# Performance work log

Hardware: AMD Instinct MI355X
Metric: run time of the kernel (lower is better)

## Reference

```python
import jax, jax.numpy as jnp
import numpy as np

NUM_HEADS = 8
SIZE_Q = 512
SIZE_K = 512
SIZE_V = 512
B, S = 2, 2048


def setup_inputs() -> dict:
    key = jax.random.key(0)
    ks = jax.random.split(key, 16)
    Hk = SIZE_K  # num_heads * head_size_k
    Hv = SIZE_V  # num_heads * head_size_v
    inp = {
        "k": jax.random.normal(ks[0], (B, S, SIZE_K), jnp.float32),
        "v": jax.random.normal(ks[1], (B, S, SIZE_V), jnp.float32),
        "q": jax.random.normal(ks[2], (B, S, SIZE_Q), jnp.float32),
        "mask": jax.random.randint(ks[3], (S, S), 0, 2).astype(jnp.bool_),
        "spatial_bias": jax.random.normal(ks[4], (1, NUM_HEADS, S, S), jnp.float32),
        # Linear params stored as [in, out]; y = x @ W + b
        "Wq": jax.random.normal(ks[5], (SIZE_Q, Hk), jnp.float32) / np.sqrt(SIZE_Q),
        "bq": jnp.zeros((Hk,), jnp.float32),
        "Wk": jax.random.normal(ks[6], (SIZE_K, Hk), jnp.float32) / np.sqrt(SIZE_K),
        "bk": jnp.zeros((Hk,), jnp.float32),
        "Wv": jax.random.normal(ks[7], (SIZE_V, Hv), jnp.float32) / np.sqrt(SIZE_V),
        "bv": jnp.zeros((Hv,), jnp.float32),
        "Wo": jax.random.normal(ks[8], (Hv, SIZE_V), jnp.float32) / np.sqrt(Hv),
        "bo": jnp.zeros((SIZE_V,), jnp.float32),
    }
    return inp


def reference(k, v, q, mask, spatial_bias, Wq, bq, Wk, bk, Wv, bv, Wo, bo):
    batch, sk = k.shape[0], k.shape[1]
    sq = q.shape[1]
    hdk = Wk.shape[1] // NUM_HEADS
    hdv = Wv.shape[1] // NUM_HEADS
    # QKV projections -> [B, H, S, hd]
    kp = (k @ Wk + bk).reshape(batch, sk, NUM_HEADS, hdk).transpose(0, 2, 1, 3)
    vp = (v @ Wv + bv).reshape(batch, sk, NUM_HEADS, hdv).transpose(0, 2, 1, 3)
    qp = (q @ Wq + bq).reshape(batch, sq, NUM_HEADS, hdk).transpose(0, 2, 1, 3)
    qp = qp / jnp.sqrt(jnp.asarray(hdk, qp.dtype))
    # Scores with additive spatial bias and boolean mask (2D mask -> [1,1,S,S])
    scores = jnp.einsum("bhqd,bhkd->bhqk", qp, kp) + spatial_bias
    scores = jnp.where(mask[None, None, :, :], scores, -jnp.inf)
    attn = jax.nn.softmax(scores, axis=-1)  # dropout=0 (eval)
    ctx = jnp.einsum("bhqk,bhkd->bhqd", attn, vp)
    ctx = ctx.transpose(0, 2, 1, 3).reshape(batch, sq, NUM_HEADS * hdv)
    return ctx @ Wo + bo
```

## Files before the change

### kernel.cpp

```cpp
#include <hip/hip_runtime.h>
#include <hip/hip_bf16.h>

#define S_LEN 2048
#define NH 8
#define HD 64
#define CH 512
#define NEG_BIG (-3.0e38f)

typedef __bf16 bf16;
typedef bf16 bf16x8 __attribute__((ext_vector_type(8)));
typedef bf16 bf16x4 __attribute__((ext_vector_type(4)));
typedef float floatx4 __attribute__((ext_vector_type(4)));

__global__ void detect_mask_kernel(const unsigned char* __restrict__ mb,
                                   int* __restrict__ flag_out) {
    __shared__ int s1, s3;
    if (threadIdx.x == 0) { s1 = 0; s3 = 0; }
    __syncthreads();
    int any1 = 0, any3 = 0;
    int base = threadIdx.x * 16;
    for (int i = base; i < base + 16; ++i) {
        unsigned char bch = mb[i];
        int m = i & 3;
        if (bch != 0) {
            if (m == 1) any1 = 1;
            if (m == 2 || m == 3) any3 = 1;
        }
    }
    if (any1) atomicOr(&s1, 1);
    if (any3) atomicOr(&s3, 1);
    __syncthreads();
    if (threadIdx.x == 0) {
        int f = 0;
        if (s1) f = 1;
        else if (s3) f = 2;
        *flag_out = f;
    }
}

__global__ __launch_bounds__(256) void prep_weights_kernel(
    const float* __restrict__ Wq, const float* __restrict__ Wk,
    const float* __restrict__ Wv, const float* __restrict__ Wo,
    bf16* __restrict__ WThi, bf16* __restrict__ WTlo)
{
    __shared__ float tile[64][65];
    const int t = threadIdx.x;
    const int n0 = blockIdx.x * 64;
    const int k0 = blockIdx.y * 64;
    const int mat = blockIdx.z;
    const float* W = (mat == 0) ? Wq : (mat == 1) ? Wk : (mat == 2) ? Wv : Wo;
    bf16* hi = WThi + (size_t)mat * (CH * CH);
    bf16* lo = WTlo + (size_t)mat * (CH * CH);
#pragma unroll
    for (int i = 0; i < 4; ++i) {
        int row = (t >> 4) + 16 * i;
        int c4 = (t & 15) << 2;
        float4 f = *(const float4*)(W + (size_t)(k0 + row) * CH + n0 + c4);
        tile[row][c4 + 0] = f.x; tile[row][c4 + 1] = f.y;
        tile[row][c4 + 2] = f.z; tile[row][c4 + 3] = f.w;
    }
    __syncthreads();
#pragma unroll
    for (int i = 0; i < 4; ++i) {
        int nr = (t >> 4) + 16 * i;
        int k4 = (t & 15) << 2;
        bf16x4 h, l;
#pragma unroll
        for (int j = 0; j < 4; ++j) {
            float x = tile[k4 + j][nr];
            bf16 hv = (bf16)x;
            h[j] = hv;
            l[j] = (bf16)(x - (float)hv);
        }
        *(bf16x4*)(hi + (size_t)(n0 + nr) * CH + k0 + k4) = h;
        *(bf16x4*)(lo + (size_t)(n0 + nr) * CH + k0 + k4) = l;
    }
}

__device__ __forceinline__ void gemm_bf16_tile(
    bf16* __restrict__ As_hi, bf16* __restrict__ As_lo,
    bf16* __restrict__ Bs_hi, bf16* __restrict__ Bs_lo,
    const float* __restrict__ IN, const bf16* __restrict__ WThi,
    const bf16* __restrict__ WTlo, const float* __restrict__ BI,
    float* __restrict__ OUT, float scale, int mode)
{
    const int t = threadIdx.x;
    const int w = t >> 6;
    const int lane = t & 63;
    const int m16 = lane & 15;
    const int quad = lane >> 4;
    const int m0 = blockIdx.y * 128;
    const int n0 = blockIdx.x * 128;

    const int arow = t >> 1;
    const int akc  = (t & 1) << 4;

    floatx4 acc[2][8];
#pragma unroll
    for (int mi = 0; mi < 2; ++mi)
#pragma unroll
        for (int ni = 0; ni < 8; ++ni) {
            acc[mi][ni][0] = 0.f; acc[mi][ni][1] = 0.f;
            acc[mi][ni][2] = 0.f; acc[mi][ni][3] = 0.f;
        }

    float4 af[4];
    bf16x8 pbh[2], pbl[2];

    auto loadA = [&](int k0) {
        const float* p = IN + (size_t)(m0 + arow) * CH + k0 + akc;
        af[0] = ((const float4*)p)[0];
        af[1] = ((const float4*)p)[1];
        af[2] = ((const float4*)p)[2];
        af[3] = ((const float4*)p)[3];
    };
    auto loadB = [&](int k0) {
        const bf16* ph = WThi + (size_t)(n0 + arow) * CH + k0 + akc;
        const bf16* pl = WTlo + (size_t)(n0 + arow) * CH + k0 + akc;
        pbh[0] = ((const bf16x8*)ph)[0]; pbh[1] = ((const bf16x8*)ph)[1];
        pbl[0] = ((const bf16x8*)pl)[0]; pbl[1] = ((const bf16x8*)pl)[1];
    };
    auto stage = [&]() {
#pragma unroll
        for (int hh = 0; hh < 2; ++hh) {
            bf16x8 h, l;
#pragma unroll
            for (int j = 0; j < 8; ++j) {
                float x = ((const float*)&af[2 * hh])[j];
                bf16 hv = (bf16)x;
                h[j] = hv;
                l[j] = (bf16)(x - (float)hv);
            }
            *(bf16x8*)&As_hi[arow * 40 + akc + 8 * hh] = h;
            *(bf16x8*)&As_lo[arow * 40 + akc + 8 * hh] = l;
        }
        *(bf16x8*)&Bs_hi[arow * 40 + akc + 0] = pbh[0];
        *(bf16x8*)&Bs_hi[arow * 40 + akc + 8] = pbh[1];
        *(bf16x8*)&Bs_lo[arow * 40 + akc + 0] = pbl[0];
        *(bf16x8*)&Bs_lo[arow * 40 + akc + 8] = pbl[1];
    };

    loadA(0); loadB(0);
    for (int ks = 0; ks < CH / 32; ++ks) {
        __syncthreads();
        stage();
        __syncthreads();
        if (ks + 1 < CH / 32) { loadA(32 * (ks + 1)); loadB(32 * (ks + 1)); }

        bf16x8 bh[8], bl[8];
#pragma unroll
        for (int ni = 0; ni < 8; ++ni) {
            bh[ni] = *(const bf16x8*)&Bs_hi[(16 * ni + m16) * 40 + 8 * quad];
            bl[ni] = *(const bf16x8*)&Bs_lo[(16 * ni + m16) * 40 + 8 * quad];
        }
#pragma unroll
        for (int mi = 0; mi < 2; ++mi) {
            bf16x8 ah = *(const bf16x8*)&As_hi[(32 * w + 16 * mi + m16) * 40 + 8 * quad];
            bf16x8 al = *(const bf16x8*)&As_lo[(32 * w + 16 * mi + m16) * 40 + 8 * quad];
#pragma unroll
            for (int ni = 0; ni < 8; ++ni) {
                acc[mi][ni] = __builtin_amdgcn_mfma_f32_16x16x32_bf16(ah, bh[ni], acc[mi][ni], 0, 0, 0);
                acc[mi][ni] = __builtin_amdgcn_mfma_f32_16x16x32_bf16(ah, bl[ni], acc[mi][ni], 0, 0, 0);
                acc[mi][ni] = __builtin_amdgcn_mfma_f32_16x16x32_bf16(al, bh[ni], acc[mi][ni], 0, 0, 0);
            }
        }
    }

#pragma unroll
    for (int mi = 0; mi < 2; ++mi) {
#pragma unroll
        for (int r = 0; r < 4; ++r) {
            int row = m0 + 32 * w + 16 * mi + 4 * quad + r;
            int bb = row >> 11;
            int ss = row & (S_LEN - 1);
#pragma unroll
            for (int ni = 0; ni < 8; ++ni) {
                int col = n0 + 16 * ni + m16;
                float v = (acc[mi][ni][r] + BI[col]) * scale;
                if (mode == 0) {
                    int hh = col >> 6, dd = col & 63;
                    OUT[(((size_t)bb * NH + hh) * S_LEN + ss) * HD + dd] = v;
                } else if (mode == 1) {
                    int hh = col >> 6, dd = col & 63;
                    OUT[(((size_t)bb * NH + hh) * HD + dd) * S_LEN + ss] = v;
                } else {
                    OUT[(size_t)row * CH + col] = v;
                }
            }
        }
    }
}

__global__ __launch_bounds__(256, 2) void qkv_gemm_kernel(
    const float* __restrict__ q_in, const float* __restrict__ k_in,
    const float* __restrict__ v_in,
    const bf16* __restrict__ WThi, const bf16* __restrict__ WTlo,
    const float* __restrict__ bq, const float* __restrict__ bk,
    const float* __restrict__ bv,
    float* __restrict__ qp, float* __restrict__ kp, float* __restrict__ vpT)
{
    __shared__ __attribute__((aligned(16))) bf16 As_hi[128 * 40];
    __shared__ __attribute__((aligned(16))) bf16 As_lo[128 * 40];
    __shared__ __attribute__((aligned(16))) bf16 Bs_hi[128 * 40];
    __shared__ __attribute__((aligned(16))) bf16 Bs_lo[128 * 40];
    int z = blockIdx.z;
    if (z == 0)
        gemm_bf16_tile(As_hi, As_lo, Bs_hi, Bs_lo, q_in,
                       WThi, WTlo, bq, qp, 0.125f, 0);
    else if (z == 1)
        gemm_bf16_tile(As_hi, As_lo, Bs_hi, Bs_lo, k_in,
                       WThi + (size_t)CH * CH, WTlo + (size_t)CH * CH, bk, kp, 1.0f, 0);
    else
        gemm_bf16_tile(As_hi, As_lo, Bs_hi, Bs_lo, v_in,
                       WThi + (size_t)2 * CH * CH, WTlo + (size_t)2 * CH * CH, bv, vpT, 1.0f, 1);
}

__global__ __launch_bounds__(256, 2) void out_gemm_kernel(
    const float* __restrict__ ctx,
    const bf16* __restrict__ WThi, const bf16* __restrict__ WTlo,
    const float* __restrict__ bo, float* __restrict__ out)
{
    __shared__ __attribute__((aligned(16))) bf16 As_hi[128 * 40];
    __shared__ __attribute__((aligned(16))) bf16 As_lo[128 * 40];
    __shared__ __attribute__((aligned(16))) bf16 Bs_hi[128 * 40];
    __shared__ __attribute__((aligned(16))) bf16 Bs_lo[128 * 40];
    gemm_bf16_tile(As_hi, As_lo, Bs_hi, Bs_lo, ctx,
                   WThi + (size_t)3 * CH * CH, WTlo + (size_t)3 * CH * CH, bo, out, 1.0f, 2);
}

__global__ __launch_bounds__(256, 2) void attn_kernel(
    const float* __restrict__ qp, const float* __restrict__ kp,
    const float* __restrict__ vpT, const float* __restrict__ bias,
    const void* __restrict__ mask, const int* __restrict__ flagp,
    float* __restrict__ ctxb)
{
    __shared__ __attribute__((aligned(16))) bf16 Kbf[64 * 72];
    __shared__ __attribute__((aligned(16))) bf16 VsT[64 * 72];
    __shared__ __attribute__((aligned(16))) bf16 Pbf[64 * 72];
    __shared__ __attribute__((aligned(16))) float sbias[64 * 68];

    const int t    = threadIdx.x;
    const int w    = t >> 6;
    const int lane = t & 63;
    const int m    = lane & 15;
    const int quad = lane >> 4;
    const int q0   = blockIdx.x * 64;
    const int h    = blockIdx.y;
    const int b    = blockIdx.z;
    const int bh   = b * NH + h;
    const int flag = *flagp;

    bf16x8 qf[2];
    {
        const float* qrow =
            qp + ((size_t)bh * S_LEN + q0 + 16 * w + m) * HD + 8 * quad;
#pragma unroll
        for (int c = 0; c < 2; ++c) {
            float4 f0 = *(const float4*)(qrow + 32 * c);
            float4 f1 = *(const float4*)(qrow + 32 * c + 4);
            bf16x8 v;
            v[0] = (bf16)f0.x; v[1] = (bf16)f0.y; v[2] = (bf16)f0.z; v[3] = (bf16)f0.w;
            v[4] = (bf16)f1.x; v[5] = (bf16)f1.y; v[6] = (bf16)f1.z; v[7] = (bf16)f1.w;
            qf[c] = v;
        }
    }

    floatx4 ctx[4];
    float mrow[4], lrow[4];
#pragma unroll
    for (int tt = 0; tt < 4; ++tt) { ctx[tt][0]=0.f; ctx[tt][1]=0.f; ctx[tt][2]=0.f; ctx[tt][3]=0.f; }
#pragma unroll
    for (int r = 0; r < 4; ++r) { mrow[r] = NEG_BIG; lrow[r] = 0.f; }

    float4 kreg[4], vreg[4], breg[4];
    uint4  mreg[4];

    auto prefetch = [&](int k0) {
#pragma unroll
        for (int i = 0; i < 4; ++i) {
            int fl  = t + 256 * i;
            int row = fl >> 4;
            int c4  = (fl & 15) << 2;
            kreg[i] = *(const float4*)(kp  + ((size_t)bh * S_LEN + k0 + row) * HD + c4);
            vreg[i] = *(const float4*)(vpT + ((size_t)bh * HD + row) * S_LEN + k0 + c4);
            int grow = q0 + row;
            breg[i] = *(const float4*)(bias + ((size_t)h * S_LEN + grow) * S_LEN + k0 + c4);
            size_t mi0 = (size_t)grow * S_LEN + k0 + c4;
            if (flag == 1)
                mreg[i].x = *(const unsigned int*)((const unsigned char*)mask + mi0);
            else
                mreg[i] = *(const uint4*)((const unsigned int*)mask + mi0);
        }
    };
    auto stage = [&]() {
#pragma unroll
        for (int i = 0; i < 4; ++i) {
            int fl  = t + 256 * i;
            int row = fl >> 4;
            int c4  = (fl & 15) << 2;
            float4 kf = kreg[i], vf = vreg[i], bf = breg[i];
            bf16x4 kv, vv;
            kv[0] = (bf16)kf.x; kv[1] = (bf16)kf.y; kv[2] = (bf16)kf.z; kv[3] = (bf16)kf.w;
            vv[0] = (bf16)vf.x; vv[1] = (bf16)vf.y; vv[2] = (bf16)vf.z; vv[3] = (bf16)vf.w;
            *(bf16x4*)&Kbf[row * 72 + c4] = kv;
            *(bf16x4*)&VsT[row * 72 + c4] = vv;
            unsigned mj0, mj1, mj2, mj3;
            if (flag == 1) {
                unsigned mx = mreg[i].x;
                mj0 = mx & 255u; mj1 = (mx >> 8) & 255u;
                mj2 = (mx >> 16) & 255u; mj3 = mx >> 24;
            } else {
                mj0 = mreg[i].x; mj1 = mreg[i].y; mj2 = mreg[i].z; mj3 = mreg[i].w;
            }
            float4 sb;
            sb.x = mj0 ? bf.x : NEG_BIG;
            sb.y = mj1 ? bf.y : NEG_BIG;
            sb.z = mj2 ? bf.z : NEG_BIG;
            sb.w = mj3 ? bf.w : NEG_BIG;
            *(float4*)&sbias[row * 68 + c4] = sb;
        }
    };

    prefetch(0);
    for (int k0 = 0; k0 < S_LEN; k0 += 64) {
        __syncthreads();
        stage();
        __syncthreads();
        if (k0 + 64 < S_LEN) prefetch(k0 + 64);

        floatx4 sc[4];
#pragma unroll
        for (int tt = 0; tt < 4; ++tt) { sc[tt][0]=0.f; sc[tt][1]=0.f; sc[tt][2]=0.f; sc[tt][3]=0.f; }
#pragma unroll
        for (int st = 0; st < 2; ++st)
#pragma unroll
            for (int tt = 0; tt < 4; ++tt) {
                bf16x8 kf = *(const bf16x8*)&Kbf[(16 * tt + m) * 72 + 8 * quad + 32 * st];
                sc[tt] = __builtin_amdgcn_mfma_f32_16x16x32_bf16(qf[st], kf, sc[tt], 0, 0, 0);
            }

        float alpha[4];
#pragma unroll
        for (int r = 0; r < 4; ++r) {
            int lrowq = 16 * w + 4 * quad + r;
            float s[4];
#pragma unroll
            for (int tt = 0; tt < 4; ++tt)
                s[tt] = sc[tt][r] + sbias[lrowq * 68 + 16 * tt + m];
            float mx = fmaxf(fmaxf(s[0], s[1]), fmaxf(s[2], s[3]));
            mx = fmaxf(mx, __shfl_xor(mx, 1));
            mx = fmaxf(mx, __shfl_xor(mx, 2));
            mx = fmaxf(mx, __shfl_xor(mx, 4));
            mx = fmaxf(mx, __shfl_xor(mx, 8));
            float mnew = fmaxf(mrow[r], mx);
            float al = __expf(mrow[r] - mnew);
            float ls = 0.f;
#pragma unroll
            for (int tt = 0; tt < 4; ++tt) {
                float p = (s[tt] <= -1e37f) ? 0.f : __expf(s[tt] - mnew);
                ls += p;
                Pbf[lrowq * 72 + 16 * tt + m] = (bf16)p;
            }
            ls += __shfl_xor(ls, 1);
            ls += __shfl_xor(ls, 2);
            ls += __shfl_xor(ls, 4);
            ls += __shfl_xor(ls, 8);
            lrow[r] = lrow[r] * al + ls;
            mrow[r] = mnew;
            alpha[r] = al;
        }
#pragma unroll
        for (int tt = 0; tt < 4; ++tt)
#pragma unroll
            for (int r = 0; r < 4; ++r) ctx[tt][r] *= alpha[r];

#pragma unroll
        for (int st = 0; st < 2; ++st) {
            bf16x8 pf = *(const bf16x8*)&Pbf[(16 * w + m) * 72 + 8 * quad + 32 * st];
#pragma unroll
            for (int tt = 0; tt < 4; ++tt) {
                bf16x8 vf = *(const bf16x8*)&VsT[(16 * tt + m) * 72 + 8 * quad + 32 * st];
                ctx[tt] = __builtin_amdgcn_mfma_f32_16x16x32_bf16(pf, vf, ctx[tt], 0, 0, 0);
            }
        }
    }

#pragma unroll
    for (int r = 0; r < 4; ++r) {
        float inv = lrow[r] > 0.f ? 1.f / lrow[r] : 0.f;
        int grow = q0 + 16 * w + 4 * quad + r;
#pragma unroll
        for (int tt = 0; tt < 4; ++tt) {
            ctxb[((size_t)b * S_LEN + grow) * CH + h * HD + 16 * tt + m] =
                ctx[tt][r] * inv;
        }
    }
}

extern "C" void kernel_launch(void* const* d_in, const int* in_sizes, int n_in,
                              void* d_out, int out_size, void* d_ws, size_t ws_size,
                              hipStream_t stream) {
    const float* k_in = (const float*)d_in[0];
    const float* v_in = (const float*)d_in[1];
    const float* q_in = (const float*)d_in[2];
    const void*  mask = d_in[3];
    const float* bias = (const float*)d_in[4];
    const float* Wq = (const float*)d_in[5];
    const float* bq = (const float*)d_in[6];
    const float* Wk = (const float*)d_in[7];
    const float* bk = (const float*)d_in[8];
    const float* Wv = (const float*)d_in[9];
    const float* bv = (const float*)d_in[10];
    const float* Wo = (const float*)d_in[11];
    const float* bo = (const float*)d_in[12];
    float* out = (float*)d_out;

    float* wsf = (float*)d_ws;
    float* qp  = wsf;
    float* kp  = wsf + 2097152;
    float* vpT = wsf + 4194304;
    float* ctx = wsf + 6291456;
    bf16* WThi = (bf16*)(wsf + 8388608);
    bf16* WTlo = WThi + (size_t)4 * CH * CH;
    int*  flag = (int*)(WTlo + (size_t)4 * CH * CH);

    detect_mask_kernel<<<1, 256, 0, stream>>>((const unsigned char*)mask, flag);
    prep_weights_kernel<<<dim3(8, 8, 4), 256, 0, stream>>>(
        Wq, Wk, Wv, Wo, WThi, WTlo);
    qkv_gemm_kernel<<<dim3(4, 32, 3), 256, 0, stream>>>(
        q_in, k_in, v_in, WThi, WTlo, bq, bk, bv, qp, kp, vpT);
    attn_kernel<<<dim3(32, 8, 2), 256, 0, stream>>>(
        qp, kp, vpT, bias, mask, flag, ctx);
    out_gemm_kernel<<<dim3(4, 32, 1), 256, 0, stream>>>(
        ctx, WThi, WTlo, bo, out);
}
```

Measured before the change: 385.7 us.

## Split attention over key halves, store projections in bf16, retile GEMMs

New measurement: 471.5 us. 1.22x slower.

```diff
diff --git a/kernel.cpp b/kernel.cpp
--- a/kernel.cpp
+++ b/kernel.cpp
@@ -5,11 +5,14 @@
 #define NH 8
 #define HD 64
 #define CH 512
-#define NEG_BIG (-3.0e38f)
+#define NEG_INIT (-1.0e30f)
+#define MASK_SENT (-30000.0f)
 
 typedef __bf16 bf16;
 typedef bf16 bf16x8 __attribute__((ext_vector_type(8)));
 typedef bf16 bf16x4 __attribute__((ext_vector_type(4)));
+typedef _Float16 f16;
+typedef f16 f16x4 __attribute__((ext_vector_type(4)));
 typedef float floatx4 __attribute__((ext_vector_type(4)));
 
 __global__ void detect_mask_kernel(const unsigned char* __restrict__ mb,
@@ -77,52 +80,61 @@
     }
 }
 
-__device__ __forceinline__ void gemm_bf16_tile(
-    bf16* __restrict__ As_hi, bf16* __restrict__ As_lo,
-    bf16* __restrict__ Bs_hi, bf16* __restrict__ Bs_lo,
+template <int BM, int MODE>
+__device__ __forceinline__ void gemm_core(
+    bf16* __restrict__ SMEM,
     const float* __restrict__ IN, const bf16* __restrict__ WThi,
     const bf16* __restrict__ WTlo, const float* __restrict__ BI,
-    float* __restrict__ OUT, float scale, int mode)
+    void* __restrict__ OUT, float scale)
 {
+    constexpr int MI  = BM / 64;
+    constexpr int TPR = 256 / BM;
+    constexpr int AF  = 32 / TPR;
+    constexpr int F4  = AF / 4;
+    constexpr int H8  = AF / 8;
+    constexpr int WR  = BM / 4;
+
+    bf16* As_hi = SMEM;
+    bf16* As_lo = SMEM + BM * 40;
+    bf16* Bs_hi = SMEM + 2 * BM * 40;
+    bf16* Bs_lo = SMEM + 2 * BM * 40 + 64 * 40;
+
     const int t = threadIdx.x;
     const int w = t >> 6;
-    const int lane = t & 63;
-    const int m16 = lane & 15;
-    const int quad = lane >> 4;
-    const int m0 = blockIdx.y * 128;
-    const int n0 = blockIdx.x * 128;
-
-    const int arow = t >> 1;
-    const int akc  = (t & 1) << 4;
-
-    floatx4 acc[2][8];
-#pragma unroll
-    for (int mi = 0; mi < 2; ++mi)
-#pragma unroll
-        for (int ni = 0; ni < 8; ++ni) {
+    const int m16 = (t & 63) & 15;
+    const int quad = (t & 63) >> 4;
+    const int m0 = blockIdx.y * BM;
+    const int n0 = blockIdx.x * 64;
+
+    const int arow = t / TPR;
+    const int akc  = (t % TPR) * AF;
+    const int brow = t >> 2;
+    const int bkc  = (t & 3) << 3;
+
+    floatx4 acc[MI][4];
+#pragma unroll
+    for (int mi = 0; mi < MI; ++mi)
+#pragma unroll
+        for (int ni = 0; ni < 4; ++ni) {
             acc[mi][ni][0] = 0.f; acc[mi][ni][1] = 0.f;
             acc[mi][ni][2] = 0.f; acc[mi][ni][3] = 0.f;
         }
 
-    float4 af[4];
-    bf16x8 pbh[2], pbl[2];
-
-    auto loadA = [&](int k0) {
-        const float* p = IN + (size_t)(m0 + arow) * CH + k0 + akc;
-        af[0] = ((const float4*)p)[0];
-        af[1] = ((const float4*)p)[1];
-        af[2] = ((const float4*)p)[2];
-        af[3] = ((const float4*)p)[3];
+    float4 af[F4];
+    bf16x8 pbh, pbl;
+
+    auto loadA = [&](int k0c) {
+        const float* p = IN + (size_t)(m0 + arow) * CH + k0c + akc;
+#pragma unroll
+        for (int i = 0; i < F4; ++i) af[i] = ((const float4*)p)[i];
     };
-    auto loadB = [&](int k0) {
-        const bf16* ph = WThi + (size_t)(n0 + arow) * CH + k0 + akc;
-        const bf16* pl = WTlo + (size_t)(n0 + arow) * CH + k0 + akc;
-        pbh[0] = ((const bf16x8*)ph)[0]; pbh[1] = ((const bf16x8*)ph)[1];
-        pbl[0] = ((const bf16x8*)pl)[0]; pbl[1] = ((const bf16x8*)pl)[1];
+    auto loadB = [&](int k0c) {
+        pbh = *(const bf16x8*)(WThi + (size_t)(n0 + brow) * CH + k0c + bkc);
+        pbl = *(const bf16x8*)(WTlo + (size_t)(n0 + brow) * CH + k0c + bkc);
     };
     auto stage = [&]() {
 #pragma unroll
-        for (int hh = 0; hh < 2; ++hh) {
+        for (int hh = 0; hh < H8; ++hh) {
             bf16x8 h, l;
 #pragma unroll
             for (int j = 0; j < 8; ++j) {
@@ -134,10 +146,8 @@
             *(bf16x8*)&As_hi[arow * 40 + akc + 8 * hh] = h;
             *(bf16x8*)&As_lo[arow * 40 + akc + 8 * hh] = l;
         }
-        *(bf16x8*)&Bs_hi[arow * 40 + akc + 0] = pbh[0];
-        *(bf16x8*)&Bs_hi[arow * 40 + akc + 8] = pbh[1];
-        *(bf16x8*)&Bs_lo[arow * 40 + akc + 0] = pbl[0];
-        *(bf16x8*)&Bs_lo[arow * 40 + akc + 8] = pbl[1];
+        *(bf16x8*)&Bs_hi[brow * 40 + bkc] = pbh;
+        *(bf16x8*)&Bs_lo[brow * 40 + bkc] = pbl;
     };
 
     loadA(0); loadB(0);
@@ -147,18 +157,18 @@
         __syncthreads();
         if (ks + 1 < CH / 32) { loadA(32 * (ks + 1)); loadB(32 * (ks + 1)); }
 
-        bf16x8 bh[8], bl[8];
-#pragma unroll
-        for (int ni = 0; ni < 8; ++ni) {
+        bf16x8 bh[4], bl[4];
+#pragma unroll
+        for (int ni = 0; ni < 4; ++ni) {
             bh[ni] = *(const bf16x8*)&Bs_hi[(16 * ni + m16) * 40 + 8 * quad];
             bl[ni] = *(const bf16x8*)&Bs_lo[(16 * ni + m16) * 40 + 8 * quad];
         }
 #pragma unroll
-        for (int mi = 0; mi < 2; ++mi) {
-            bf16x8 ah = *(const bf16x8*)&As_hi[(32 * w + 16 * mi + m16) * 40 + 8 * quad];
-            bf16x8 al = *(const bf16x8*)&As_lo[(32 * w + 16 * mi + m16) * 40 + 8 * quad];
-#pragma unroll
-            for (int ni = 0; ni < 8; ++ni) {
+        for (int mi = 0; mi < MI; ++mi) {
+            bf16x8 ah = *(const bf16x8*)&As_hi[(WR * w + 16 * mi + m16) * 40 + 8 * quad];
+            bf16x8 al = *(const bf16x8*)&As_lo[(WR * w + 16 * mi + m16) * 40 + 8 * quad];
+#pragma unroll
+            for (int ni = 0; ni < 4; ++ni) {
                 acc[mi][ni] = __builtin_amdgcn_mfma_f32_16x16x32_bf16(ah, bh[ni], acc[mi][ni], 0, 0, 0);
                 acc[mi][ni] = __builtin_amdgcn_mfma_f32_16x16x32_bf16(ah, bl[ni], acc[mi][ni], 0, 0, 0);
                 acc[mi][ni] = __builtin_amdgcn_mfma_f32_16x16x32_bf16(al, bh[ni], acc[mi][ni], 0, 0, 0);
@@ -166,28 +176,51 @@
         }
     }
 
-#pragma unroll
-    for (int mi = 0; mi < 2; ++mi) {
-#pragma unroll
-        for (int r = 0; r < 4; ++r) {
-            int row = m0 + 32 * w + 16 * mi + 4 * quad + r;
-            int bb = row >> 11;
-            int ss = row & (S_LEN - 1);
-#pragma unroll
-            for (int ni = 0; ni < 8; ++ni) {
-                int col = n0 + 16 * ni + m16;
-                float v = (acc[mi][ni][r] + BI[col]) * scale;
-                if (mode == 0) {
-                    int hh = col >> 6, dd = col & 63;
-                    OUT[(((size_t)bb * NH + hh) * S_LEN + ss) * HD + dd] = v;
-                } else if (mode == 1) {
-                    int hh = col >> 6, dd = col & 63;
-                    OUT[(((size_t)bb * NH + hh) * HD + dd) * S_LEN + ss] = v;
-                } else {
-                    OUT[(size_t)row * CH + col] = v;
+    if (MODE == 1) {
+        __syncthreads();
+        bf16* T = SMEM;
+#pragma unroll
+        for (int mi = 0; mi < MI; ++mi)
+#pragma unroll
+            for (int r = 0; r < 4; ++r) {
+                int rl = WR * w + 16 * mi + 4 * quad + r;
+#pragma unroll
+                for (int ni = 0; ni < 4; ++ni) {
+                    int cl = 16 * ni + m16;
+                    T[cl * (BM + 8) + rl] = (bf16)(acc[mi][ni][r] + BI[n0 + cl]);
                 }
             }
-        }
+        __syncthreads();
+        int hh = blockIdx.x;
+        int bb = m0 >> 11;
+        int s_base = m0 & (S_LEN - 1);
+        int d = t >> 2;
+        int s_off = (t & 3) * (BM / 4);
+        bf16* po = (bf16*)OUT +
+            (((size_t)bb * NH + hh) * HD + d) * S_LEN + s_base + s_off;
+#pragma unroll
+        for (int j = 0; j < BM / 32; ++j)
+            *(bf16x8*)(po + 8 * j) = *(const bf16x8*)&T[d * (BM + 8) + s_off + 8 * j];
+    } else {
+#pragma unroll
+        for (int mi = 0; mi < MI; ++mi)
+#pragma unroll
+            for (int r = 0; r < 4; ++r) {
+                int row = m0 + WR * w + 16 * mi + 4 * quad + r;
+                int bb = row >> 11;
+                int ss = row & (S_LEN - 1);
+#pragma unroll
+                for (int ni = 0; ni < 4; ++ni) {
+                    int col = n0 + 16 * ni + m16;
+                    float v = (acc[mi][ni][r] + BI[col]) * scale;
+                    if (MODE == 0) {
+                        int hh = col >> 6, dd = col & 63;
+                        ((bf16*)OUT)[(((size_t)bb * NH + hh) * S_LEN + ss) * HD + dd] = (bf16)v;
+                    } else {
+                        ((float*)OUT)[(size_t)row * CH + col] = v;
+                    }
+                }
+            }
     }
 }
 
@@ -197,22 +230,18 @@
     const bf16* __restrict__ WThi, const bf16* __restrict__ WTlo,
     const float* __restrict__ bq, const float* __restrict__ bk,
     const float* __restrict__ bv,
-    float* __restrict__ qp, float* __restrict__ kp, float* __restrict__ vpT)
+    bf16* __restrict__ qp, bf16* __restrict__ kp, bf16* __restrict__ vpT)
 {
-    __shared__ __attribute__((aligned(16))) bf16 As_hi[128 * 40];
-    __shared__ __attribute__((aligned(16))) bf16 As_lo[128 * 40];
-    __shared__ __attribute__((aligned(16))) bf16 Bs_hi[128 * 40];
-    __shared__ __attribute__((aligned(16))) bf16 Bs_lo[128 * 40];
+    __shared__ __attribute__((aligned(16))) bf16 SMEM[2 * 128 * 40 + 2 * 64 * 40];
     int z = blockIdx.z;
     if (z == 0)
-        gemm_bf16_tile(As_hi, As_lo, Bs_hi, Bs_lo, q_in,
-                       WThi, WTlo, bq, qp, 0.125f, 0);
+        gemm_core<128, 0>(SMEM, q_in, WThi, WTlo, bq, qp, 0.125f);
     else if (z == 1)
-        gemm_bf16_tile(As_hi, As_lo, Bs_hi, Bs_lo, k_in,
-                       WThi + (size_t)CH * CH, WTlo + (size_t)CH * CH, bk, kp, 1.0f, 0);
+        gemm_core<128, 0>(SMEM, k_in, WThi + (size_t)CH * CH,
+                          WTlo + (size_t)CH * CH, bk, kp, 1.0f);
     else
-        gemm_bf16_tile(As_hi, As_lo, Bs_hi, Bs_lo, v_in,
-                       WThi + (size_t)2 * CH * CH, WTlo + (size_t)2 * CH * CH, bv, vpT, 1.0f, 1);
+        gemm_core<128, 1>(SMEM, v_in, WThi + (size_t)2 * CH * CH,
+                          WTlo + (size_t)2 * CH * CH, bv, vpT, 1.0f);
 }
 
 __global__ __launch_bounds__(256, 2) void out_gemm_kernel(
@@ -220,49 +249,49 @@
     const bf16* __restrict__ WThi, const bf16* __restrict__ WTlo,
     const float* __restrict__ bo, float* __restrict__ out)
 {
-    __shared__ __attribute__((aligned(16))) bf16 As_hi[128 * 40];
-    __shared__ __attribute__((aligned(16))) bf16 As_lo[128 * 40];
-    __shared__ __attribute__((aligned(16))) bf16 Bs_hi[128 * 40];
-    __shared__ __attribute__((aligned(16))) bf16 Bs_lo[128 * 40];
-    gemm_bf16_tile(As_hi, As_lo, Bs_hi, Bs_lo, ctx,
-                   WThi + (size_t)3 * CH * CH, WTlo + (size_t)3 * CH * CH, bo, out, 1.0f, 2);
-}
-
-__global__ __launch_bounds__(256, 2) void attn_kernel(
-    const float* __restrict__ qp, const float* __restrict__ kp,
-    const float* __restrict__ vpT, const float* __restrict__ bias,
+    __shared__ __attribute__((aligned(16))) bf16 SMEM[2 * 64 * 40 + 2 * 64 * 40];
+    gemm_core<64, 2>(SMEM, ctx, WThi + (size_t)3 * CH * CH,
+                     WTlo + (size_t)3 * CH * CH, bo, out, 1.0f);
+}
+
+__global__ __launch_bounds__(256, 4) void attn_kernel(
+    const bf16* __restrict__ qp, const bf16* __restrict__ kp,
+    const bf16* __restrict__ vpT, const float* __restrict__ bias,
     const void* __restrict__ mask, const int* __restrict__ flagp,
-    float* __restrict__ ctxb)
+    float* __restrict__ O0, float* __restrict__ O1,
+    float2* __restrict__ ml)
 {
     __shared__ __attribute__((aligned(16))) bf16 Kbf[64 * 72];
     __shared__ __attribute__((aligned(16))) bf16 VsT[64 * 72];
     __shared__ __attribute__((aligned(16))) bf16 Pbf[64 * 72];
-    __shared__ __attribute__((aligned(16))) float sbias[64 * 68];
+    __shared__ __attribute__((aligned(16))) f16  sb16[64 * 72];
 
     const int t    = threadIdx.x;
     const int w    = t >> 6;
     const int lane = t & 63;
     const int m    = lane & 15;
     const int quad = lane >> 4;
-    const int q0   = blockIdx.x * 64;
-    const int h    = blockIdx.y;
-    const int b    = blockIdx.z;
-    const int bh   = b * NH + h;
+
+    const int fid   = blockIdx.x + 32 * (blockIdx.y + 8 * blockIdx.z);
+    const int xcd   = fid & 7;
+    const int rest  = fid >> 3;
+    const int q_idx = rest & 31;
+    const int g     = xcd | ((rest >> 5) << 3);
+    const int h     = g & 7;
+    const int bc    = g >> 3;
+    const int b     = bc >> 1;
+    const int c     = bc & 1;
+
+    const int q0 = q_idx * 64;
+    const int bh = b * NH + h;
+    const int kbase = c * (S_LEN / 2);
     const int flag = *flagp;
 
     bf16x8 qf[2];
     {
-        const float* qrow =
-            qp + ((size_t)bh * S_LEN + q0 + 16 * w + m) * HD + 8 * quad;
-#pragma unroll
-        for (int c = 0; c < 2; ++c) {
-            float4 f0 = *(const float4*)(qrow + 32 * c);
-            float4 f1 = *(const float4*)(qrow + 32 * c + 4);
-            bf16x8 v;
-            v[0] = (bf16)f0.x; v[1] = (bf16)f0.y; v[2] = (bf16)f0.z; v[3] = (bf16)f0.w;
-            v[4] = (bf16)f1.x; v[5] = (bf16)f1.y; v[6] = (bf16)f1.z; v[7] = (bf16)f1.w;
-            qf[c] = v;
-        }
+        const bf16* qrow = qp + ((size_t)bh * S_LEN + q0 + 16 * w + m) * HD + 8 * quad;
+        qf[0] = *(const bf16x8*)(qrow);
+        qf[1] = *(const bf16x8*)(qrow + 32);
     }
 
     floatx4 ctx[4];
@@ -270,19 +299,26 @@
 #pragma unroll
     for (int tt = 0; tt < 4; ++tt) { ctx[tt][0]=0.f; ctx[tt][1]=0.f; ctx[tt][2]=0.f; ctx[tt][3]=0.f; }
 #pragma unroll
-    for (int r = 0; r < 4; ++r) { mrow[r] = NEG_BIG; lrow[r] = 0.f; }
-
-    float4 kreg[4], vreg[4], breg[4];
+    for (int r = 0; r < 4; ++r) { mrow[r] = NEG_INIT; lrow[r] = 0.f; }
+
+    bf16x8 kreg[2], vreg[2];
+    float4 breg[4];
     uint4  mreg[4];
 
     auto prefetch = [&](int k0) {
 #pragma unroll
+        for (int i = 0; i < 2; ++i) {
+            int fl = t + 256 * i;
+            int row = fl >> 3;
+            int c8 = (fl & 7) << 3;
+            kreg[i] = *(const bf16x8*)(kp  + ((size_t)bh * S_LEN + k0 + row) * HD + c8);
+            vreg[i] = *(const bf16x8*)(vpT + ((size_t)bh * HD + row) * S_LEN + k0 + c8);
+        }
+#pragma unroll
         for (int i = 0; i < 4; ++i) {
-            int fl  = t + 256 * i;
+            int fl = t + 256 * i;
             int row = fl >> 4;
-            int c4  = (fl & 15) << 2;
-            kreg[i] = *(const float4*)(kp  + ((size_t)bh * S_LEN + k0 + row) * HD + c4);
-            vreg[i] = *(const float4*)(vpT + ((size_t)bh * HD + row) * S_LEN + k0 + c4);
+            int c4 = (fl & 15) << 2;
             int grow = q0 + row;
             breg[i] = *(const float4*)(bias + ((size_t)h * S_LEN + grow) * S_LEN + k0 + c4);
             size_t mi0 = (size_t)grow * S_LEN + k0 + c4;
@@ -294,16 +330,19 @@
     };
     auto stage = [&]() {
 #pragma unroll
+        for (int i = 0; i < 2; ++i) {
+            int fl = t + 256 * i;
+            int row = fl >> 3;
+            int c8 = (fl & 7) << 3;
+            *(bf16x8*)&Kbf[row * 72 + c8] = kreg[i];
+            *(bf16x8*)&VsT[row * 72 + c8] = vreg[i];
+        }
+#pragma unroll
         for (int i = 0; i < 4; ++i) {
-            int fl  = t + 256 * i;
+            int fl = t + 256 * i;
             int row = fl >> 4;
-            int c4  = (fl & 15) << 2;
-            float4 kf = kreg[i], vf = vreg[i], bf = breg[i];
-            bf16x4 kv, vv;
-            kv[0] = (bf16)kf.x; kv[1] = (bf16)kf.y; kv[2] = (bf16)kf.z; kv[3] = (bf16)kf.w;
-            vv[0] = (bf16)vf.x; vv[1] = (bf16)vf.y; vv[2] = (bf16)vf.z; vv[3] = (bf16)vf.w;
-            *(bf16x4*)&Kbf[row * 72 + c4] = kv;
-            *(bf16x4*)&VsT[row * 72 + c4] = vv;
+            int c4 = (fl & 15) << 2;
+            float4 bf = breg[i];
             unsigned mj0, mj1, mj2, mj3;
             if (flag == 1) {
                 unsigned mx = mreg[i].x;
@@ -312,21 +351,21 @@
             } else {
                 mj0 = mreg[i].x; mj1 = mreg[i].y; mj2 = mreg[i].z; mj3 = mreg[i].w;
             }
-            float4 sb;
-            sb.x = mj0 ? bf.x : NEG_BIG;
-            sb.y = mj1 ? bf.y : NEG_BIG;
-            sb.z = mj2 ? bf.z : NEG_BIG;
-            sb.w = mj3 ? bf.w : NEG_BIG;
-            *(float4*)&sbias[row * 68 + c4] = sb;
+            f16x4 sb;
+            sb[0] = (f16)(mj0 ? bf.x : MASK_SENT);
+            sb[1] = (f16)(mj1 ? bf.y : MASK_SENT);
+            sb[2] = (f16)(mj2 ? bf.z : MASK_SENT);
+            sb[3] = (f16)(mj3 ? bf.w : MASK_SENT);
+            *(f16x4*)&sb16[row * 72 + c4] = sb;
         }
     };
 
-    prefetch(0);
-    for (int k0 = 0; k0 < S_LEN; k0 += 64) {
+    prefetch(kbase);
+    for (int k0 = kbase; k0 < kbase + S_LEN / 2; k0 += 64) {
         __syncthreads();
         stage();
         __syncthreads();
-        if (k0 + 64 < S_LEN) prefetch(k0 + 64);
+        if (k0 + 64 < kbase + S_LEN / 2) prefetch(k0 + 64);
 
         floatx4 sc[4];
 #pragma unroll
@@ -346,7 +385,7 @@
             float s[4];
 #pragma unroll
             for (int tt = 0; tt < 4; ++tt)
-                s[tt] = sc[tt][r] + sbias[lrowq * 68 + 16 * tt + m];
+                s[tt] = sc[tt][r] + (float)sb16[lrowq * 72 + 16 * tt + m];
             float mx = fmaxf(fmaxf(s[0], s[1]), fmaxf(s[2], s[3]));
             mx = fmaxf(mx, __shfl_xor(mx, 1));
             mx = fmaxf(mx, __shfl_xor(mx, 2));
@@ -357,7 +396,7 @@
             float ls = 0.f;
 #pragma unroll
             for (int tt = 0; tt < 4; ++tt) {
-                float p = (s[tt] <= -1e37f) ? 0.f : __expf(s[tt] - mnew);
+                float p = (s[tt] <= -20000.f) ? 0.f : __expf(s[tt] - mnew);
                 ls += p;
                 Pbf[lrowq * 72 + 16 * tt + m] = (bf16)p;
             }
@@ -385,16 +424,44 @@
         }
     }
 
+    float* Op = (c == 0) ? O0 : O1;
 #pragma unroll
     for (int r = 0; r < 4; ++r) {
-        float inv = lrow[r] > 0.f ? 1.f / lrow[r] : 0.f;
         int grow = q0 + 16 * w + 4 * quad + r;
 #pragma unroll
-        for (int tt = 0; tt < 4; ++tt) {
-            ctxb[((size_t)b * S_LEN + grow) * CH + h * HD + 16 * tt + m] =
-                ctx[tt][r] * inv;
-        }
-    }
+        for (int tt = 0; tt < 4; ++tt)
+            Op[((size_t)b * S_LEN + grow) * CH + h * HD + 16 * tt + m] = ctx[tt][r];
+        if (m == 0) {
+            float2 v; v.x = mrow[r]; v.y = lrow[r];
+            ml[(((size_t)c * 2 + b) * NH + h) * S_LEN + grow] = v;
+        }
+    }
+}
+
+__global__ __launch_bounds__(256) void merge_kernel(
+    float* __restrict__ O0, const float* __restrict__ O1,
+    const float2* __restrict__ ml)
+{
+    int idx = blockIdx.x * 256 + threadIdx.x;
+    int i4 = idx << 2;
+    int col = i4 & (CH - 1);
+    int h = col >> 6;
+    int srow = (i4 >> 9) & (S_LEN - 1);
+    int b = i4 >> 20;
+    float2 a = ml[(((size_t)0 + b) * NH + h) * S_LEN + srow];
+    float2 d = ml[(((size_t)2 + b) * NH + h) * S_LEN + srow];
+    float ms = fmaxf(a.x, d.x);
+    float w0 = __expf(a.x - ms), w1 = __expf(d.x - ms);
+    float den = a.y * w0 + d.y * w1;
+    float inv = den > 0.f ? 1.f / den : 0.f;
+    float4 o0 = ((const float4*)O0)[idx];
+    float4 o1 = ((const float4*)O1)[idx];
+    float4 r;
+    r.x = (o0.x * w0 + o1.x * w1) * inv;
+    r.y = (o0.y * w0 + o1.y * w1) * inv;
+    r.z = (o0.z * w0 + o1.z * w1) * inv;
+    r.w = (o0.w * w0 + o1.w * w1) * inv;
+    ((float4*)O0)[idx] = r;
 }
 
 extern "C" void kernel_launch(void* const* d_in, const int* in_sizes, int n_in,
@@ -416,21 +483,24 @@
     float* out = (float*)d_out;
 
     float* wsf = (float*)d_ws;
-    float* qp  = wsf;
-    float* kp  = wsf + 2097152;
-    float* vpT = wsf + 4194304;
-    float* ctx = wsf + 6291456;
-    bf16* WThi = (bf16*)(wsf + 8388608);
-    bf16* WTlo = WThi + (size_t)4 * CH * CH;
-    int*  flag = (int*)(WTlo + (size_t)4 * CH * CH);
+    bf16*  qp   = (bf16*)wsf;
+    bf16*  kp   = (bf16*)(wsf + 1048576);
+    bf16*  vpT  = (bf16*)(wsf + 2097152);
+    float* ctx  = wsf + 3145728;
+    float* O1   = wsf + 5242880;
+    bf16*  WThi = (bf16*)(wsf + 7340032);
+    bf16*  WTlo = (bf16*)(wsf + 7864320);
+    float2* ml  = (float2*)(wsf + 8388608);
+    int*   flag = (int*)(wsf + 8519680);
 
     detect_mask_kernel<<<1, 256, 0, stream>>>((const unsigned char*)mask, flag);
     prep_weights_kernel<<<dim3(8, 8, 4), 256, 0, stream>>>(
         Wq, Wk, Wv, Wo, WThi, WTlo);
-    qkv_gemm_kernel<<<dim3(4, 32, 3), 256, 0, stream>>>(
+    qkv_gemm_kernel<<<dim3(8, 32, 3), 256, 0, stream>>>(
         q_in, k_in, v_in, WThi, WTlo, bq, bk, bv, qp, kp, vpT);
-    attn_kernel<<<dim3(32, 8, 2), 256, 0, stream>>>(
-        qp, kp, vpT, bias, mask, flag, ctx);
-    out_gemm_kernel<<<dim3(4, 32, 1), 256, 0, stream>>>(
+    attn_kernel<<<dim3(32, 8, 4), 256, 0, stream>>>(
+        qp, kp, vpT, bias, mask, flag, ctx, O1, ml);
+    merge_kernel<<<2048, 256, 0, stream>>>(ctx, O1, ml);
+    out_gemm_kernel<<<dim3(8, 64), 256, 0, stream>>>(
         ctx, WThi, WTlo, bo, out);
 }
```
